# Performance work log

Hardware: AMD Instinct MI355X
Metric: run time of the kernel (lower is better)

## Reference

```python
import jax, jax.numpy as jnp
import numpy as np

H = 192; W = 192; A = 9; STRIDE = 16; NUM_GT = 128
IM_H = H * STRIDE; IM_W = W * STRIDE
RPN_NEG = 0.3; RPN_POS = 0.7; RPN_BATCH = 256; NUM_FG = int(0.5 * RPN_BATCH)


def _base_anchors(base_size=16, ratios=(0.5, 1.0, 2.0), scales=(8, 16, 32)):
    cx = cy = (base_size - 1) / 2.0
    size = float(base_size * base_size)
    out = []
    for r in ratios:
        ws = np.round(np.sqrt(size / r)); hs = np.round(ws * r)
        for s in scales:
            w = ws * s; h = hs * s
            out.append([cx - 0.5 * (w - 1), cy - 0.5 * (h - 1), cx + 0.5 * (w - 1), cy + 0.5 * (h - 1)])
    return np.asarray(out, dtype=np.float32)


def setup_inputs() -> dict:
    key = jax.random.key(0)
    k1, k2, k3 = jax.random.split(key, 3)
    base = _base_anchors()
    sx = np.arange(W, dtype=np.float32) * STRIDE
    sy = np.arange(H, dtype=np.float32) * STRIDE
    xs, ys = np.meshgrid(sx, sy)
    shifts = np.stack([xs.ravel(), ys.ravel(), xs.ravel(), ys.ravel()], axis=1).astype(np.float32)
    all_anchors = (shifts[:, None, :] + base[None, :, :]).reshape(-1, 4)  # [N,4]
    # gt boxes: valid x1y1x2y2 inside the image, plus class col
    xy = jax.random.uniform(k1, (NUM_GT, 2)) * jnp.array([IM_W - 320.0, IM_H - 320.0])
    wh = 32.0 + jax.random.uniform(k2, (NUM_GT, 2)) * 256.0
    gt_boxes = jnp.concatenate([xy, xy + wh, jnp.ones((NUM_GT, 1))], axis=1).astype(jnp.float32)
    rpn_cls_score = jax.random.normal(k3, (1, H, W, 2 * A), dtype=jnp.float32)
    im_info = jnp.array([IM_H, IM_W, 1.0], dtype=jnp.float32)
    return {"rpn_cls_score": rpn_cls_score, "gt_boxes": gt_boxes, "im_info": im_info,
            "all_anchors": jnp.asarray(all_anchors)}


def _iou(anchors, gt):  # [N,4] x [G,4] -> [N,G], Pascal +1 convention
    ax1, ay1, ax2, ay2 = (anchors[:, i:i + 1] for i in range(4))
    gx1, gy1, gx2, gy2 = (gt[None, :, i] for i in range(4))
    iw = jnp.clip(jnp.minimum(ax2, gx2) - jnp.maximum(ax1, gx1) + 1.0, 0.0)
    ih = jnp.clip(jnp.minimum(ay2, gy2) - jnp.maximum(ay1, gy1) + 1.0, 0.0)
    inter = iw * ih
    aa = (ax2 - ax1 + 1.0) * (ay2 - ay1 + 1.0)
    ga = (gx2 - gx1 + 1.0) * (gy2 - gy1 + 1.0)
    return inter / (aa + ga - inter)


def _bbox_transform(ex, gt):  # encode gt relative to ex anchors, [N,4]
    ew = ex[:, 2] - ex[:, 0] + 1.0; eh = ex[:, 3] - ex[:, 1] + 1.0
    ecx = ex[:, 0] + 0.5 * ew;      ecy = ex[:, 1] + 0.5 * eh
    gw = gt[:, 2] - gt[:, 0] + 1.0; gh = gt[:, 3] - gt[:, 1] + 1.0
    gcx = gt[:, 0] + 0.5 * gw;      gcy = gt[:, 1] + 0.5 * gh
    return jnp.stack([(gcx - ecx) / ew, (gcy - ecy) / eh, jnp.log(gw / ew), jnp.log(gh / eh)], axis=1)


def reference(rpn_cls_score, gt_boxes, im_info, all_anchors):
    N = all_anchors.shape[0]
    h = rpn_cls_score.shape[1]; w = rpn_cls_score.shape[2]
    # inside-image mask replaces the dynamic-shape gather/unmap of the TF code
    inside = ((all_anchors[:, 0] >= 0.0) & (all_anchors[:, 1] >= 0.0) &
              (all_anchors[:, 2] < im_info[1]) & (all_anchors[:, 3] < im_info[0]))
    ov = _iou(all_anchors, gt_boxes[:, :4])                 # [N,G]
    mov = jnp.where(inside[:, None], ov, -1.0)
    max_ov = jnp.max(mov, axis=1)                           # per-anchor best overlap
    argmax = jnp.argmax(ov, axis=1)                         # per-anchor best gt
    gt_max = jnp.max(mov, axis=0)                           # per-gt best overlap
    is_best = inside & jnp.any(mov == gt_max[None, :], axis=1)

    labels = jnp.full((N,), -1.0, dtype=jnp.float32)
    labels = jnp.where(inside & (max_ov < RPN_NEG), 0.0, labels)
    # TF code sets best-anchor-per-gt label to -1 * old label (quirk kept faithfully)
    labels = jnp.where(is_best, -labels, labels)
    labels = jnp.where(inside & (max_ov >= RPN_POS), 1.0, labels)

    # fg/bg subsampling via random ranking (deterministic key; TF used tf.random.shuffle)
    key = jax.random.key(42)
    kf, kb = jax.random.split(key)
    fg = labels == 1.0
    rf = jnp.where(fg, jax.random.uniform(kf, (N,)), 2.0)
    rankf = jnp.argsort(jnp.argsort(rf))
    labels = jnp.where(fg & (rankf >= NUM_FG), -1.0, labels)
    num_bg = RPN_BATCH - jnp.sum((labels == 1.0).astype(jnp.int32))
    bg = labels == 0.0
    rb = jnp.where(bg, jax.random.uniform(kb, (N,)), 2.0)
    rankb = jnp.argsort(jnp.argsort(rb))
    labels = jnp.where(bg & (rankb >= num_bg), -1.0, labels)

    targets = _bbox_transform(all_anchors, gt_boxes[argmax, :4])
    targets = jnp.where(inside[:, None], targets, 0.0)

    ones4 = jnp.ones((1, 4), dtype=jnp.float32)
    inside_w = jnp.where((labels == 1.0)[:, None], 1.0, 0.0) * ones4
    num_ex = jnp.sum((labels >= 0.0).astype(jnp.float32))
    outside_w = jnp.where(((labels == 1.0) | (labels == 0.0))[:, None], 1.0 / num_ex, 0.0) * ones4

    rpn_labels = labels.reshape(1, h, w, A).astype(jnp.int32)
    rpn_bbox_targets = targets.reshape(1, h, w, A * 4)
    rpn_bbox_inside_weights = inside_w.reshape(1, h, w, A * 4)
    rpn_bbox_outside_weights = outside_w.reshape(1, h, w, A * 4)
    return (rpn_labels, rpn_bbox_targets, rpn_bbox_inside_weights, rpn_bbox_outside_weights)
```

## Files before the change

### kernel.cpp

```cpp
#include <hip/hip_runtime.h>
#include <stdint.h>

#define TF_PARTITIONABLE 1

#define GMAX 128
#define FG_CAP 8192
#define BGC_CAP 8192
#define LDS_CAP 2048
#define T1 0.00390625f
#define RPN_NEG 0.3f
#define RPN_POS 0.7f

struct U2 { uint32_t a, b; };

__host__ __device__ constexpr U2 tf2x32(uint32_t k0, uint32_t k1, uint32_t x0, uint32_t x1) {
  uint32_t ks2 = k0 ^ k1 ^ 0x1BD11BDAu;
  x0 += k0; x1 += k1;
#define TFR(r) { x0 += x1; x1 = (uint32_t)((x1 << (r)) | (x1 >> (32 - (r)))); x1 ^= x0; }
  TFR(13) TFR(15) TFR(26) TFR(6)
  x0 += k1; x1 += ks2 + 1u;
  TFR(17) TFR(29) TFR(16) TFR(24)
  x0 += ks2; x1 += k0 + 2u;
  TFR(13) TFR(15) TFR(26) TFR(6)
  x0 += k0; x1 += k1 + 3u;
  TFR(17) TFR(29) TFR(16) TFR(24)
  x0 += k1; x1 += ks2 + 4u;
  TFR(13) TFR(15) TFR(26) TFR(6)
  x0 += ks2; x1 += k0 + 5u;
#undef TFR
  return U2{x0, x1};
}

#if TF_PARTITIONABLE
constexpr U2 KEYF = tf2x32(0u, 42u, 0u, 0u);
constexpr U2 KEYB = tf2x32(0u, 42u, 0u, 1u);
#else
constexpr U2 C02 = tf2x32(0u, 42u, 0u, 2u);
constexpr U2 C13 = tf2x32(0u, 42u, 1u, 3u);
constexpr U2 KEYF = U2{C02.a, C13.a};
constexpr U2 KEYB = U2{C02.b, C13.b};
#endif

__device__ __forceinline__ float tf_uniform(uint32_t k0, uint32_t k1, uint32_t i, uint32_t N) {
#if TF_PARTITIONABLE
  U2 r = tf2x32(k0, k1, 0u, i);
  uint32_t bits = r.a ^ r.b;
#else
  uint32_t h = N >> 1;
  uint32_t bits;
  if (i < h) { U2 r = tf2x32(k0, k1, i, i + h); bits = r.a; }
  else       { U2 r = tf2x32(k0, k1, i - h, i); bits = r.b; }
#endif
  return __uint_as_float((bits >> 9) | 0x3f800000u) - 1.0f;
}

__device__ __forceinline__ void window(float4 B, float gx1, float gy1, float gx2, float gy2,
                                       int W, int H, int& c0, int& c1, int& r0, int& r1) {
  c0 = (int)floorf((gx1 - 1.0f - B.z) * 0.0625f) - 1; if (c0 < 0) c0 = 0;
  c1 = (int)ceilf ((gx2 + 1.0f - B.x) * 0.0625f) + 1; if (c1 > W - 1) c1 = W - 1;
  r0 = (int)floorf((gy1 - 1.0f - B.w) * 0.0625f) - 1; if (r0 < 0) r0 = 0;
  r1 = (int)ceilf ((gy2 + 1.0f - B.y) * 0.0625f) + 1; if (r1 > H - 1) r1 = H - 1;
}

__device__ __forceinline__ uint32_t waveAppend(uint32_t* lds_cnt, bool pred) {
  unsigned long long m = __ballot(pred);
  uint32_t my = 0u;
  if (m) {
    int lane = (int)(threadIdx.x & 63);
    int lead = __ffsll(m) - 1;
    uint32_t rank = (uint32_t)__popcll(m & ((1ull << lane) - 1ull));
    uint32_t base = 0u;
    if (lane == lead) base = atomicAdd(lds_cnt, (uint32_t)__popcll(m));
    base = __shfl(base, lead);
    my = base + rank;
  }
  return my;
}


__global__ __launch_bounds__(256) void k_pre2(const float4* __restrict__ anchors,
    const float* __restrict__ gt, const float* __restrict__ im_info,
    int W, int H, int A, int G,
    float* __restrict__ gt_max_s, uint32_t* __restrict__ scalars) {
#pragma clang fp contract(off)
  int t = threadIdx.x;
  if (blockIdx.x == (unsigned)(G * A)) {
    if (t < 32) scalars[t] = 0u;
    return;
  }
  int g = blockIdx.x / A, s = blockIdx.x % A;
  float4 B = anchors[s];
  float gx1 = gt[g*5], gy1 = gt[g*5+1], gx2 = gt[g*5+2], gy2 = gt[g*5+3];
  float ga = (gx2 - gx1 + 1.0f) * (gy2 - gy1 + 1.0f);
  float aa = (B.z - B.x + 1.0f) * (B.w - B.y + 1.0f);
  float imH = im_info[0], imW = im_info[1];
  int c0, c1, r0, r1;
  window(B, gx1, gy1, gx2, gy2, W, H, c0, c1, r0, r1);
  float m = -1.0f;
  if (c1 >= c0 && r1 >= r0) {
    int wc = c1 - c0 + 1, tot = wc * (r1 - r0 + 1);
    for (int idx = t; idx < tot; idx += 256) {
      int row = r0 + idx / wc, col = c0 + idx % wc;
      float fx = 16.0f * (float)col, fy = 16.0f * (float)row;
      float ax = B.x + fx, ay = B.y + fy, az = B.z + fx, aw = B.w + fy;
      if (!(ax >= 0.0f && ay >= 0.0f && az < imW && aw < imH)) continue;
      float iwr = fminf(az, gx2) - fmaxf(ax, gx1) + 1.0f;
      float ihr = fminf(aw, gy2) - fmaxf(ay, gy1) + 1.0f;
      if (iwr > 0.0f && ihr > 0.0f) {
        float inter = iwr * ihr;
        m = fmaxf(m, inter / ((aa + ga) - inter));
      }
    }
  }
#pragma unroll
  for (int d = 1; d < 64; d <<= 1) m = fmaxf(m, __shfl_xor(m, d));
  __shared__ float wm[4];
  if ((t & 63) == 0) wm[t >> 6] = m;
  __syncthreads();
  if (t == 0)
    gt_max_s[blockIdx.x] = fmaxf(fmaxf(wm[0], wm[1]), fmaxf(wm[2], wm[3]));
}

__global__ __launch_bounds__(256) void k_work(const float4* __restrict__ anchors,
    const float* __restrict__ gt, const float* __restrict__ im_info,
    int W, int H, int A, int G, int N, int ntx,
    int* __restrict__ amax, int8_t* __restrict__ label,
    const float* __restrict__ gt_max_s, uint32_t* __restrict__ scalars,
    int* __restrict__ fgIdx, float* __restrict__ fgVal,
    int* __restrict__ bgcIdx, float* __restrict__ bgcVal) {
#pragma clang fp contract(off)
  __shared__ float4 sgt4[GMAX];
  __shared__ float sga[GMAX];
  __shared__ float sgm[GMAX];
  __shared__ int slist[GMAX];
  __shared__ float4 sB[3];
  __shared__ float sBa[3];
  __shared__ float4 sBu;
  __shared__ uint32_t wcnt[4];
  __shared__ uint32_t lcnt[3], lbase[2];
  int t = threadIdx.x;
  int tile = blockIdx.x / 3, sg = blockIdx.x % 3;
  int tc = tile % ntx, tr = tile / ntx;
  float imH = im_info[0], imW = im_info[1];
  if (t < 3) {
    lcnt[t] = 0u;
    float4 bb = anchors[sg * 3 + t];
    sB[t] = bb;
    sBa[t] = (bb.z - bb.x + 1.0f) * (bb.w - bb.y + 1.0f);
  }
  if (t == 0) {
    float4 u = anchors[0];
    for (int s = 1; s < A; ++s) {
      float4 bb = anchors[s];
      u.x = fminf(u.x, bb.x); u.y = fminf(u.y, bb.y);
      u.z = fmaxf(u.z, bb.z); u.w = fmaxf(u.w, bb.w);
    }
    sBu = u;
  }
  __syncthreads();
  bool fl = false;
  if (t < G) {
    int c0, c1, r0, r1;
    window(sBu, gt[t*5], gt[t*5+1], gt[t*5+2], gt[t*5+3], W, H, c0, c1, r0, r1);
    fl = (c1 >= c0 && r1 >= r0 &&
          c0 <= tc*16+15 && c1 >= tc*16 && r0 <= tr*16+15 && r1 >= tr*16);
  }
  unsigned long long bm = __ballot(fl);
  int wv = t >> 6, ln = t & 63;
  if (ln == 0) wcnt[wv] = (uint32_t)__popcll(bm);
  __syncthreads();
  int cnt = (int)(wcnt[0] + wcnt[1]);
  if (fl) {
    uint32_t base = (wv == 1) ? wcnt[0] : 0u;
    uint32_t rank = (uint32_t)__popcll(bm & ((1ull << ln) - 1ull));
    slist[base + rank] = t;
  }
  __syncthreads();
  for (int q = t; q < cnt; q += 256) {
    int g = slist[q];
    float x1 = gt[g*5], y1 = gt[g*5+1], x2 = gt[g*5+2], y2 = gt[g*5+3];
    sgt4[q] = make_float4(x1, y1, x2, y2);
    sga[q] = (x2 - x1 + 1.0f) * (y2 - y1 + 1.0f);
    float gm = gt_max_s[g * A];
    for (int s = 1; s < A; ++s) gm = fmaxf(gm, gt_max_s[g * A + s]);
    sgm[q] = gm;
  }
  __syncthreads();

  int col = tc * 16 + (t & 15), row = tr * 16 + (t >> 4);
  bool validCell = (col < W) && (row < H);
  float fx = 16.0f * (float)col, fy = 16.0f * (float)row;
  if (!validCell) { fx = -1.0e9f; fy = -1.0e9f; }
  float ax[3], ay[3], az[3], aw[3], aab[3], best[3];
  int am[3];
  bool tie[3] = {false, false, false};
  uint32_t insM = 0u;
#pragma unroll
  for (int k = 0; k < 3; ++k) {
    float4 bb = sB[k];
    ax[k] = bb.x + fx; ay[k] = bb.y + fy;
    az[k] = bb.z + fx; aw[k] = bb.w + fy;
    aab[k] = sBa[k];
    if (ax[k] >= 0.0f && ay[k] >= 0.0f && az[k] < imW && aw[k] < imH) insM |= 1u << k;
    best[k] = 0.0f; am[k] = 0;
  }
  for (int q = 0; q < cnt; ++q) {
    float4 G4 = sgt4[q];
    float ga = sga[q];
    float gm = sgm[q];
    int g = slist[q];
#pragma unroll
    for (int k = 0; k < 3; ++k) {
      float iwr = fminf(az[k], G4.z) - fmaxf(ax[k], G4.x) + 1.0f;
      float ihr = fminf(aw[k], G4.w) - fmaxf(ay[k], G4.y) + 1.0f;
      float inter = fmaxf(iwr, 0.0f) * fmaxf(ihr, 0.0f);
      float v = inter / ((aab[k] + ga) - inter);
      if (v > best[k]) { best[k] = v; am[k] = g; }
      tie[k] |= (v == gm);
    }
  }
  int clsA[3]; float valA[3]; uint32_t myA[3];
#pragma unroll
  for (int k = 0; k < 3; ++k) {
    int s = sg * 3 + k;
    int i = (row * W + col) * A + s;
    bool ins = (insM >> k) & 1u;
    int lab = -1;
    if (ins) {
      if (best[k] < RPN_NEG) lab = 0;
      if (tie[k]) lab = -lab;
      if (best[k] >= RPN_POS) lab = 1;
    }
    bool isf = validCell && (lab == 1);
    bool isb = validCell && (lab == 0);
    if (validCell) { label[i] = (int8_t)lab; amax[i] = am[k]; }
    float val = 0.0f;
    if (isf) val = tf_uniform(KEYF.a, KEYF.b, (uint32_t)i, (uint32_t)N);
    if (isb) val = tf_uniform(KEYB.a, KEYB.b, (uint32_t)i, (uint32_t)N);
    bool cand = isb && (val < T1);
    unsigned long long mb = __ballot(isb);
    if ((t & 63) == 0 && mb) atomicAdd(&lcnt[2], (uint32_t)__popcll(mb));
    uint32_t mf = waveAppend(&lcnt[0], isf);
    uint32_t mc = waveAppend(&lcnt[1], cand);
    clsA[k] = isf ? 0 : (cand ? 1 : -1);
    valA[k] = val;
    myA[k] = isf ? mf : mc;
  }
  __syncthreads();
  if (t == 0) {
    lbase[0] = lcnt[0] ? atomicAdd(&scalars[0], lcnt[0]) : 0u;
    lbase[1] = lcnt[1] ? atomicAdd(&scalars[2], lcnt[1]) : 0u;
    if (lcnt[2]) atomicAdd(&scalars[1], lcnt[2]);
  }
  __syncthreads();
#pragma unroll
  for (int k = 0; k < 3; ++k) {
    int s = sg * 3 + k;
    int i = (row * W + col) * A + s;
    if (clsA[k] == 0) {
      uint32_t p = lbase[0] + myA[k];
      if (p < FG_CAP) { fgIdx[p] = i; fgVal[p] = valA[k]; }
    } else if (clsA[k] == 1) {
      uint32_t p = lbase[1] + myA[k];
      if (p < BGC_CAP) { bgcIdx[p] = i; bgcVal[p] = valA[k]; }
    }
  }
}

__global__ __launch_bounds__(256) void k_output(const float4* __restrict__ anchors,
    const float* __restrict__ gt, const float* __restrict__ im_info, int N,
    const int* __restrict__ amax, const int8_t* __restrict__ label,
    const uint32_t* __restrict__ scalars,
    const int* __restrict__ fgIdx, const float* __restrict__ fgVal,
    const int* __restrict__ bgcIdx, const float* __restrict__ bgcVal,
    float* __restrict__ out) {
#pragma clang fp contract(off)
  __shared__ float lv[LDS_CAP];
  __shared__ int   li[LDS_CAP];
  __shared__ uint32_t hist[256];
  __shared__ int binT; __shared__ uint32_t baseT;
  __shared__ int mcnt;
  __shared__ float mv[256]; __shared__ int mi[256]; __shared__ uint32_t mr[256];
  __shared__ float s_cv[2]; __shared__ int s_ci[2]; __shared__ float s_inv;
  int t = threadIdx.x;
  uint32_t F = scalars[0], B = scalars[1];
  uint32_t k_f = F > 128u ? 128u : F;
  uint32_t k_b = 256u - k_f;
  if (t == 0) {
    uint32_t kept = k_f + (B < k_b ? B : k_b);
    s_inv = kept ? (1.0f / (float)kept) : 0.0f;
    s_cv[0] = __uint_as_float(0x7f800000u); s_ci[0] = 0x7fffffff;
    s_cv[1] = __uint_as_float(0x7f800000u); s_ci[1] = 0x7fffffff;
  }
  __syncthreads();
  for (int pass = 0; pass < 2; ++pass) {
    const float* gvals = pass ? bgcVal : fgVal;
    const int*   gidxs = pass ? bgcIdx : fgIdx;
    uint32_t tot = pass ? B : F;
    uint32_t kk  = pass ? k_b : k_f;
    uint32_t rawn = pass ? scalars[2] : F;
    uint32_t cap  = pass ? (uint32_t)BGC_CAP : (uint32_t)FG_CAP;
    int n = (int)(rawn > cap ? cap : rawn);
    float scale = pass ? (256.0f / T1) : 256.0f;
    bool need = (tot > kk) && (kk > 0u) && ((uint32_t)n >= kk);
    bool useLds = need && (n <= LDS_CAP);
    if (useLds)
      for (int j = t; j < n; j += 256) { lv[j] = gvals[j]; li[j] = gidxs[j]; }
    const float* vals = useLds ? (const float*)lv : gvals;
    const int*   idxs = useLds ? (const int*)li : gidxs;
    hist[t] = 0u;
    if (t == 0) { mcnt = 0; binT = -1; baseT = 0u; }
    __syncthreads();
    if (need)
      for (int j = t; j < n; j += 256) {
        int b = (int)(vals[j] * scale); if (b > 255) b = 255;
        atomicAdd(&hist[b], 1u);
      }
    __syncthreads();
    if (need && t == 0) {
      uint32_t c = 0;
      for (int b = 0; b < 256; ++b) {
        if (c + hist[b] >= kk) { binT = b; baseT = c; break; }
        c += hist[b];
      }
    }
    __syncthreads();
    if (need)
      for (int j = t; j < n; j += 256) {
        int b = (int)(vals[j] * scale); if (b > 255) b = 255;
        if (b == binT) {
          int p = atomicAdd(&mcnt, 1);
          if (p < 256) { mv[p] = vals[j]; mi[p] = idxs[j]; }
        }
      }
    __syncthreads();
    int m = mcnt > 256 ? 256 : mcnt;
    if (t < m) mr[t] = baseT;
    __syncthreads();
    if (need)
      for (int j = t; j < n; j += 256) {
        float v = vals[j]; int i = idxs[j];
        int b = (int)(v * scale); if (b > 255) b = 255;
        if (b == binT)
          for (int q = 0; q < m; ++q)
            if (v < mv[q] || (v == mv[q] && i < mi[q])) atomicAdd(&mr[q], 1u);
      }
    __syncthreads();
    if (need && t < m && mr[t] == kk - 1u) { s_cv[pass] = mv[t]; s_ci[pass] = mi[t]; }
    __syncthreads();
  }

  float invw = s_inv;
  float cvF = s_cv[0]; int ciF = s_ci[0];
  float cvB = s_cv[1]; int ciB = s_ci[1];
  int i = blockIdx.x * 256 + t;
  if (i >= N) return;
  float4 a = anchors[i];
  float imH = im_info[0], imW = im_info[1];
  bool inside = (a.x >= 0.0f && a.y >= 0.0f && a.z < imW && a.w < imH);
  int lab = label[i];
  if (lab == 1) {
    float v = tf_uniform(KEYF.a, KEYF.b, (uint32_t)i, (uint32_t)N);
    if (!(v < cvF || (v == cvF && i <= ciF))) lab = -1;
  } else if (lab == 0) {
    float v = tf_uniform(KEYB.a, KEYB.b, (uint32_t)i, (uint32_t)N);
    if (!(v < cvB || (v == cvB && i <= ciB))) lab = -1;
  }
  out[i] = (float)lab;
  float4 tt = make_float4(0.0f, 0.0f, 0.0f, 0.0f);
  if (inside) {
    int g = amax[i];
    float gx1 = gt[g*5], gy1 = gt[g*5+1], gx2 = gt[g*5+2], gy2 = gt[g*5+3];
    float ew = a.z - a.x + 1.0f, eh = a.w - a.y + 1.0f;
    float ecx = a.x + 0.5f * ew, ecy = a.y + 0.5f * eh;
    float gw = gx2 - gx1 + 1.0f, gh = gy2 - gy1 + 1.0f;
    float gcx = gx1 + 0.5f * gw, gcy = gy1 + 0.5f * gh;
    tt.x = (gcx - ecx) / ew;
    tt.y = (gcy - ecy) / eh;
    tt.z = logf(gw / ew);
    tt.w = logf(gh / eh);
  }
  ((float4*)(out + (size_t)N))[i] = tt;
  float iw = (lab == 1) ? 1.0f : 0.0f;
  ((float4*)(out + 5 * (size_t)N))[i] = make_float4(iw, iw, iw, iw);
  float ow = (lab == 0 || lab == 1) ? invw : 0.0f;
  ((float4*)(out + 9 * (size_t)N))[i] = make_float4(ow, ow, ow, ow);
}

extern "C" void kernel_launch(void* const* d_in, const int* in_sizes, int n_in,
                              void* d_out, int out_size, void* d_ws, size_t ws_size,
                              hipStream_t stream) {
  const float* gt      = (const float*)d_in[1];
  const float* im_info = (const float*)d_in[2];
  const float4* anchors = (const float4*)d_in[3];
  int N = in_sizes[3] / 4;
  int G = in_sizes[1] / 5;
  if (G > GMAX) G = GMAX;
  const int A = 9;
  int HW = N / A;
  int W = (int)(sqrtf((float)HW) + 0.5f);
  int H = HW / W;
  int ntx = (W + 15) / 16, nty = (H + 15) / 16;
  int ntiles = ntx * nty;
  int nGather = ntiles * 3;
  float* out = (float*)d_out;

  uint8_t* w = (uint8_t*)d_ws;
  uint32_t* scalars  = (uint32_t*)w;
  float*    gt_max_s = (float*)(w + 4096);
  int*      amax     = (int*)(w + 16384);
  int8_t*   label    = (int8_t*)(w + 16384 + (size_t)N * 4);

  int*   fgIdx  = (int*)(out + (size_t)N);
  float* fgVal  = (float*)(out + 2 * (size_t)N);
  int*   bgcIdx = (int*)(out + 3 * (size_t)N);
  float* bgcVal = (float*)(out + 4 * (size_t)N);

  int nb = (N + 255) / 256;
  k_pre2<<<G * A + 1, 256, 0, stream>>>(anchors, gt, im_info, W, H, A, G,
                                        gt_max_s, scalars);
  k_work<<<nGather, 256, 0, stream>>>(anchors, gt, im_info, W, H, A, G, N, ntx,
                                      amax, label, gt_max_s, scalars,
                                      fgIdx, fgVal, bgcIdx, bgcVal);
  k_output<<<nb, 256, 0, stream>>>(anchors, gt, im_info, N, amax, label, scalars,
                                   fgIdx, fgVal, bgcIdx, bgcVal, out);
}
```

Before: 45.91 us.

## Split k_work into one block per anchor shape with per-shape GT culling

```diff
diff --git a/kernel.cpp b/kernel.cpp
--- a/kernel.cpp
+++ b/kernel.cpp
@@ -133,35 +133,20 @@
   __shared__ float sga[GMAX];
   __shared__ float sgm[GMAX];
   __shared__ int slist[GMAX];
-  __shared__ float4 sB[3];
-  __shared__ float sBa[3];
-  __shared__ float4 sBu;
   __shared__ uint32_t wcnt[4];
   __shared__ uint32_t lcnt[3], lbase[2];
   int t = threadIdx.x;
-  int tile = blockIdx.x / 3, sg = blockIdx.x % 3;
+  int tile = blockIdx.x / A, s = blockIdx.x % A;
   int tc = tile % ntx, tr = tile / ntx;
   float imH = im_info[0], imW = im_info[1];
-  if (t < 3) {
-    lcnt[t] = 0u;
-    float4 bb = anchors[sg * 3 + t];
-    sB[t] = bb;
-    sBa[t] = (bb.z - bb.x + 1.0f) * (bb.w - bb.y + 1.0f);
-  }
-  if (t == 0) {
-    float4 u = anchors[0];
-    for (int s = 1; s < A; ++s) {
-      float4 bb = anchors[s];
-      u.x = fminf(u.x, bb.x); u.y = fminf(u.y, bb.y);
-      u.z = fmaxf(u.z, bb.z); u.w = fmaxf(u.w, bb.w);
-    }
-    sBu = u;
-  }
+  if (t < 3) lcnt[t] = 0u;
+  float4 B = anchors[s];
+  float aab = (B.z - B.x + 1.0f) * (B.w - B.y + 1.0f);
   __syncthreads();
   bool fl = false;
   if (t < G) {
     int c0, c1, r0, r1;
-    window(sBu, gt[t*5], gt[t*5+1], gt[t*5+2], gt[t*5+3], W, H, c0, c1, r0, r1);
+    window(B, gt[t*5], gt[t*5+1], gt[t*5+2], gt[t*5+3], W, H, c0, c1, r0, r1);
     fl = (c1 >= c0 && r1 >= r0 &&
           c0 <= tc*16+15 && c1 >= tc*16 && r0 <= tr*16+15 && r1 >= tr*16);
   }
@@ -182,7 +167,7 @@
     sgt4[q] = make_float4(x1, y1, x2, y2);
     sga[q] = (x2 - x1 + 1.0f) * (y2 - y1 + 1.0f);
     float gm = gt_max_s[g * A];
-    for (int s = 1; s < A; ++s) gm = fmaxf(gm, gt_max_s[g * A + s]);
+    for (int s2 = 1; s2 < A; ++s2) gm = fmaxf(gm, gt_max_s[g * A + s2]);
     sgm[q] = gm;
   }
   __syncthreads();
@@ -191,61 +176,42 @@
   bool validCell = (col < W) && (row < H);
   float fx = 16.0f * (float)col, fy = 16.0f * (float)row;
   if (!validCell) { fx = -1.0e9f; fy = -1.0e9f; }
-  float ax[3], ay[3], az[3], aw[3], aab[3], best[3];
-  int am[3];
-  bool tie[3] = {false, false, false};
-  uint32_t insM = 0u;
-#pragma unroll
-  for (int k = 0; k < 3; ++k) {
-    float4 bb = sB[k];
-    ax[k] = bb.x + fx; ay[k] = bb.y + fy;
-    az[k] = bb.z + fx; aw[k] = bb.w + fy;
-    aab[k] = sBa[k];
-    if (ax[k] >= 0.0f && ay[k] >= 0.0f && az[k] < imW && aw[k] < imH) insM |= 1u << k;
-    best[k] = 0.0f; am[k] = 0;
-  }
+  float ax = B.x + fx, ay = B.y + fy;
+  float az = B.z + fx, aw = B.w + fy;
+  bool ins = (ax >= 0.0f && ay >= 0.0f && az < imW && aw < imH);
+  float best = 0.0f;
+  int am = 0;
+  bool tie = false;
   for (int q = 0; q < cnt; ++q) {
     float4 G4 = sgt4[q];
     float ga = sga[q];
     float gm = sgm[q];
     int g = slist[q];
-#pragma unroll
-    for (int k = 0; k < 3; ++k) {
-      float iwr = fminf(az[k], G4.z) - fmaxf(ax[k], G4.x) + 1.0f;
-      float ihr = fminf(aw[k], G4.w) - fmaxf(ay[k], G4.y) + 1.0f;
-      float inter = fmaxf(iwr, 0.0f) * fmaxf(ihr, 0.0f);
-      float v = inter / ((aab[k] + ga) - inter);
-      if (v > best[k]) { best[k] = v; am[k] = g; }
-      tie[k] |= (v == gm);
-    }
-  }
-  int clsA[3]; float valA[3]; uint32_t myA[3];
-#pragma unroll
-  for (int k = 0; k < 3; ++k) {
-    int s = sg * 3 + k;
-    int i = (row * W + col) * A + s;
-    bool ins = (insM >> k) & 1u;
-    int lab = -1;
-    if (ins) {
-      if (best[k] < RPN_NEG) lab = 0;
-      if (tie[k]) lab = -lab;
-      if (best[k] >= RPN_POS) lab = 1;
-    }
-    bool isf = validCell && (lab == 1);
-    bool isb = validCell && (lab == 0);
-    if (validCell) { label[i] = (int8_t)lab; amax[i] = am[k]; }
-    float val = 0.0f;
-    if (isf) val = tf_uniform(KEYF.a, KEYF.b, (uint32_t)i, (uint32_t)N);
-    if (isb) val = tf_uniform(KEYB.a, KEYB.b, (uint32_t)i, (uint32_t)N);
-    bool cand = isb && (val < T1);
-    unsigned long long mb = __ballot(isb);
-    if ((t & 63) == 0 && mb) atomicAdd(&lcnt[2], (uint32_t)__popcll(mb));
-    uint32_t mf = waveAppend(&lcnt[0], isf);
-    uint32_t mc = waveAppend(&lcnt[1], cand);
-    clsA[k] = isf ? 0 : (cand ? 1 : -1);
-    valA[k] = val;
-    myA[k] = isf ? mf : mc;
-  }
+    float iwr = fminf(az, G4.z) - fmaxf(ax, G4.x) + 1.0f;
+    float ihr = fminf(aw, G4.w) - fmaxf(ay, G4.y) + 1.0f;
+    float inter = fmaxf(iwr, 0.0f) * fmaxf(ihr, 0.0f);
+    float v = inter / ((aab + ga) - inter);
+    if (v > best) { best = v; am = g; }
+    tie |= (v == gm);
+  }
+  int i = (row * W + col) * A + s;
+  int lab = -1;
+  if (ins) {
+    if (best < RPN_NEG) lab = 0;
+    if (tie) lab = -lab;
+    if (best >= RPN_POS) lab = 1;
+  }
+  bool isf = validCell && (lab == 1);
+  bool isb = validCell && (lab == 0);
+  if (validCell) { label[i] = (int8_t)lab; amax[i] = am; }
+  float val = 0.0f;
+  if (isf) val = tf_uniform(KEYF.a, KEYF.b, (uint32_t)i, (uint32_t)N);
+  if (isb) val = tf_uniform(KEYB.a, KEYB.b, (uint32_t)i, (uint32_t)N);
+  bool cand = isb && (val < T1);
+  unsigned long long mb = __ballot(isb);
+  if ((t & 63) == 0 && mb) atomicAdd(&lcnt[2], (uint32_t)__popcll(mb));
+  uint32_t mf = waveAppend(&lcnt[0], isf);
+  uint32_t mc = waveAppend(&lcnt[1], cand);
   __syncthreads();
   if (t == 0) {
     lbase[0] = lcnt[0] ? atomicAdd(&scalars[0], lcnt[0]) : 0u;
@@ -253,17 +219,12 @@
     if (lcnt[2]) atomicAdd(&scalars[1], lcnt[2]);
   }
   __syncthreads();
-#pragma unroll
-  for (int k = 0; k < 3; ++k) {
-    int s = sg * 3 + k;
-    int i = (row * W + col) * A + s;
-    if (clsA[k] == 0) {
-      uint32_t p = lbase[0] + myA[k];
-      if (p < FG_CAP) { fgIdx[p] = i; fgVal[p] = valA[k]; }
-    } else if (clsA[k] == 1) {
-      uint32_t p = lbase[1] + myA[k];
-      if (p < BGC_CAP) { bgcIdx[p] = i; bgcVal[p] = valA[k]; }
-    }
+  if (isf) {
+    uint32_t p = lbase[0] + mf;
+    if (p < FG_CAP) { fgIdx[p] = i; fgVal[p] = val; }
+  } else if (cand) {
+    uint32_t p = lbase[1] + mc;
+    if (p < BGC_CAP) { bgcIdx[p] = i; bgcVal[p] = val; }
   }
 }
 
@@ -402,7 +363,7 @@
   int H = HW / W;
   int ntx = (W + 15) / 16, nty = (H + 15) / 16;
   int ntiles = ntx * nty;
-  int nGather = ntiles * 3;
+  int nGather = ntiles * A;
   float* out = (float*)d_out;
 
   uint8_t* w = (uint8_t*)d_ws;
```

Measured after the change: 55.76 us. 21.5% more time.
